# Performance work log

Measured on AMD Instinct MI355X. Metric: run time of the kernel, lower is better.

## Reference

```python
import jax, jax.numpy as jnp
import numpy as np

N = 50000   # num_nodes
E = 800000  # num_edges
IN, HID, OUT = 64, 96, 96
LN_EPS = 1e-5


def setup_inputs() -> dict:
    key = jax.random.key(0)
    ks = jax.random.split(key, 12)
    s = 0.05
    return {
        "x": jax.random.normal(ks[0], (N, IN), jnp.float32),
        "edge_index": jax.random.randint(ks[1], (2, E), 0, N, dtype=jnp.int64),
        "edge_weight": jax.random.uniform(ks[2], (E,), jnp.float32),
        "W0": jax.random.normal(ks[3], (IN, HID), jnp.float32) * s,
        "b0": jnp.zeros((HID,), jnp.float32),
        "ln_g": jnp.ones((HID,), jnp.float32),
        "ln_b": jnp.zeros((HID,), jnp.float32),
        "Ws": jax.random.normal(ks[4], (IN, HID), jnp.float32) * s,
        "bs": jnp.zeros((HID,), jnp.float32),
        "W1": jax.random.normal(ks[5], (HID, OUT), jnp.float32) * s,
        "b1": jnp.zeros((OUT,), jnp.float32),
    }


def _gcn(h, W, b, src, dst, ew, n):
    # GCNConv with add_self_loops=True and edge weights (PyG gcn_norm)
    loop = jnp.arange(n, dtype=src.dtype)
    s = jnp.concatenate([src, loop])
    d = jnp.concatenate([dst, loop])
    w = jnp.concatenate([ew, jnp.ones((n,), ew.dtype)])
    deg = jax.ops.segment_sum(w, d, num_segments=n)
    dinv = jnp.where(deg > 0, jax.lax.rsqrt(jnp.maximum(deg, 1e-12)), 0.0)
    norm = dinv[s] * w * dinv[d]                 # [E+N]
    msg = (h @ W)[s] * norm[:, None]             # gather transformed src feats
    return jax.ops.segment_sum(msg, d, num_segments=n) + b


def _layernorm(h, g, b):
    mu = h.mean(-1, keepdims=True)
    var = ((h - mu) ** 2).mean(-1, keepdims=True)
    return (h - mu) * jax.lax.rsqrt(var + LN_EPS) * g + b


def reference(x, edge_index, edge_weight, W0, b0, ln_g, ln_b, Ws, bs, W1, b1):
    src, dst = edge_index[0], edge_index[1]
    n = x.shape[0]
    # layer 0: GCN -> LayerNorm -> ReLU -> (dropout: eval no-op) -> +Linear skip
    h = _gcn(x, W0, b0, src, dst, edge_weight, n)
    h = jax.nn.relu(_layernorm(h, ln_g, ln_b))
    h = h + (x @ Ws + bs)
    # final layer: GCN only
    return _gcn(h, W1, b1, src, dst, edge_weight, n)
```

## Files before the change

### kernel.cpp

```cpp
#include <hip/hip_runtime.h>

#define LN_EPS 1e-5f

__device__ __forceinline__ float bflo(unsigned u) { union { unsigned u; float f; } c; c.u = u << 16; return c.f; }
__device__ __forceinline__ float bfhi(unsigned u) { union { unsigned u; float f; } c; c.u = u & 0xffff0000u; return c.f; }
__device__ __forceinline__ unsigned f2bfbits(float f) {
    union { float f; unsigned u; } c; c.f = f;
    return (c.u + 0x7fffu + ((c.u >> 16) & 1u)) >> 16;
}
__device__ __forceinline__ unsigned packbf(float lo, float hi) {
    return f2bfbits(lo) | (f2bfbits(hi) << 16);
}

__global__ void cnt_rank_kernel(const int* __restrict__ dst, int* __restrict__ cnt,
                                int* __restrict__ rank, int e) {
    int i = blockIdx.x * 256 + threadIdx.x;
    if (i >= e) return;
    rank[i] = atomicAdd(&cnt[dst[i]], 1);
}

__global__ void cvtprep_kernel(const float* __restrict__ x, unsigned* __restrict__ xb2, int total4,
                               const float* __restrict__ W0, const float* __restrict__ Ws,
                               const float* __restrict__ W1,
                               float4* __restrict__ w0i, float4* __restrict__ wsi,
                               float4* __restrict__ w1i, int* __restrict__ cnt,
                               int n, int gX) {
    int b = (int)blockIdx.x;
    if (b < gX) {
        int i = b * 256 + threadIdx.x;
        if (i >= total4) return;
        float4 v = ((const float4*)x)[i];
        uint2 o;
        o.x = packbf(v.x, v.y);
        o.y = packbf(v.z, v.w);
        ((uint2*)xb2)[i] = o;
    } else if (b < gX + 15) {
        int i = (b - gX) * 256 + threadIdx.x;
        if (i < 1536) {
            int kq = i / 96, j = i % 96;
            const float* p = W0 + kq * 4 * 96 + j;
            w0i[i] = make_float4(p[0], p[96], p[192], p[288]);
            const float* q = Ws + kq * 4 * 96 + j;
            wsi[i] = make_float4(q[0], q[96], q[192], q[288]);
        }
        int i2 = i - 1536;
        if (i2 >= 0 && i2 < 2304) {
            int kq = i2 / 96, j = i2 % 96;
            const float* p = W1 + kq * 4 * 96 + j;
            w1i[i2] = make_float4(p[0], p[96], p[192], p[288]);
        }
    } else {
        int i4 = ((b - gX - 15) * 256 + threadIdx.x) * 4;
        if (i4 + 3 < n) *(int4*)(cnt + i4) = make_int4(0, 0, 0, 0);
        else for (int k = i4; k < n; ++k) cnt[k] = 0;
    }
}

__global__ void blocksum_kernel(const int* __restrict__ cnt, int* __restrict__ bsum, int n) {
    int base = blockIdx.x * 1024;
    int t = threadIdx.x;
    int i0 = base + t * 4;
    int s = 0;
    if (i0 + 3 < n) { int4 v = *(const int4*)(cnt + i0); s = v.x + v.y + v.z + v.w; }
    else { for (int k = 0; k < 4; ++k) if (i0 + k < n) s += cnt[i0 + k]; }
    #pragma unroll
    for (int off = 32; off; off >>= 1) s += __shfl_xor(s, off);
    __shared__ int wsum[4];
    if ((t & 63) == 0) wsum[t >> 6] = s;
    __syncthreads();
    if (t == 0) bsum[blockIdx.x] = wsum[0] + wsum[1] + wsum[2] + wsum[3];
}

__global__ void scan_bsum_kernel(const int* __restrict__ bsum, int* __restrict__ boff, int nb) {
    int t = threadIdx.x;
    int carry = 0;
    for (int base = 0; base < nb; base += 64) {
        int i = base + t;
        int v = (i < nb) ? bsum[i] : 0;
        int sc = v;
        #pragma unroll
        for (int off = 1; off < 64; off <<= 1) {
            int u = __shfl_up(sc, off);
            if (t >= off) sc += u;
        }
        if (i < nb) boff[i] = carry + sc - v;
        carry += __shfl(sc, 63);
    }
}

__global__ void rowptr_kernel(const int* __restrict__ cnt, const int* __restrict__ boff,
                              int* __restrict__ rowptr, int n, int etot) {
    __shared__ int wsum[4];
    int b = blockIdx.x;
    int t = threadIdx.x;
    int i0 = b * 1024 + t * 4;
    int c0 = 0, c1 = 0, c2 = 0, c3 = 0;
    if (i0 < n)     c0 = cnt[i0];
    if (i0 + 1 < n) c1 = cnt[i0 + 1];
    if (i0 + 2 < n) c2 = cnt[i0 + 2];
    if (i0 + 3 < n) c3 = cnt[i0 + 3];
    int tot = c0 + c1 + c2 + c3;
    int lane = t & 63, w = t >> 6;
    int sc = tot;
    #pragma unroll
    for (int off = 1; off < 64; off <<= 1) {
        int u = __shfl_up(sc, off);
        if (lane >= off) sc += u;
    }
    if (lane == 63) wsum[w] = sc;
    __syncthreads();
    int woff = 0;
    for (int k = 0; k < w; ++k) woff += wsum[k];
    int excl = boff[b] + woff + sc - tot;
    if (i0 < n)     rowptr[i0]     = excl;
    if (i0 + 1 < n) rowptr[i0 + 1] = excl + c0;
    if (i0 + 2 < n) rowptr[i0 + 2] = excl + c0 + c1;
    if (i0 + 3 < n) rowptr[i0 + 3] = excl + c0 + c1 + c2;
    if (b == 0 && t == 0) rowptr[n] = etot;
}

__global__ void scatter_part_kernel(const int* __restrict__ src, const int* __restrict__ dst,
                                    const float* __restrict__ ew, const int* __restrict__ rank,
                                    const int* __restrict__ rowptr,
                                    uint2* __restrict__ cv, int e, int n) {
    int part = blockIdx.x & 7;
    int blk  = blockIdx.x >> 3;
    int chunk = (n + 7) >> 3;
    int lo = part * chunk;
    int hi = lo + chunk; if (hi > n) hi = n;
    int stride = (gridDim.x >> 3) * 256;
    for (int i = blk * 256 + threadIdx.x; i < e; i += stride) {
        int d = dst[i];
        if (d >= lo && d < hi) {
            int pos = rowptr[d] + rank[i];
            cv[pos] = make_uint2((unsigned)src[i], __float_as_uint(ew[i]));
        }
    }
}

__global__ void degsum_kernel(const int* __restrict__ rowptr, const uint2* __restrict__ cv,
                              float* __restrict__ dinv, int n) {
    int i = blockIdx.x * 256 + threadIdx.x;
    if (i >= n) return;
    int p0 = rowptr[i], p1 = rowptr[i + 1];
    float s = 1.0f;
    for (int p = p0; p < p1; ++p) s += __uint_as_float(cv[p].y);
    dinv[i] = rsqrtf(s);
}

__global__ void agg64_kernel(const unsigned* __restrict__ xb, const float* __restrict__ dinv,
                             const int* __restrict__ rowptr, const uint2* __restrict__ cv,
                             float* __restrict__ aggX, int n) {
    int node = blockIdx.x * 4 + (threadIdx.x >> 6);
    if (node >= n) return;
    int lane = threadIdx.x & 63;
    int g = lane >> 4, l4 = lane & 15;
    const uint2* x2 = (const uint2*)xb;
    int p0 = rowptr[node], pe = rowptr[node + 1];
    float a0 = 0, a1 = 0, a2 = 0, a3 = 0;
    float b0 = 0, b1 = 0, b2 = 0, b3 = 0;
    for (int p = p0 + g; p < pe; p += 8) {
        uint2 e1 = cv[p];
        int s1 = (int)e1.x;
        float w1 = __uint_as_float(e1.y) * dinv[s1];
        uint2 r1 = x2[(size_t)s1 * 16 + l4];
        bool h2 = (p + 4) < pe;
        uint2 e2 = h2 ? cv[p + 4] : e1;
        int s2 = (int)e2.x;
        float w2 = h2 ? __uint_as_float(e2.y) * dinv[s2] : 0.0f;
        uint2 r2 = x2[(size_t)s2 * 16 + l4];
        a0 = fmaf(w1, bflo(r1.x), a0); a1 = fmaf(w1, bfhi(r1.x), a1);
        a2 = fmaf(w1, bflo(r1.y), a2); a3 = fmaf(w1, bfhi(r1.y), a3);
        b0 = fmaf(w2, bflo(r2.x), b0); b1 = fmaf(w2, bfhi(r2.x), b1);
        b2 = fmaf(w2, bflo(r2.y), b2); b3 = fmaf(w2, bfhi(r2.y), b3);
    }
    a0 += b0; a1 += b1; a2 += b2; a3 += b3;
    #pragma unroll
    for (int off = 16; off <= 32; off <<= 1) {
        a0 += __shfl_xor(a0, off);
        a1 += __shfl_xor(a1, off);
        a2 += __shfl_xor(a2, off);
        a3 += __shfl_xor(a3, off);
    }
    if (g == 0) {
        float di = dinv[node];
        uint2 sr = x2[(size_t)node * 16 + l4];
        a0 = fmaf(di, bflo(sr.x), a0); a1 = fmaf(di, bfhi(sr.x), a1);
        a2 = fmaf(di, bflo(sr.y), a2); a3 = fmaf(di, bfhi(sr.y), a3);
        ((float4*)(aggX + (size_t)node * 64))[l4] =
            make_float4(a0 * di, a1 * di, a2 * di, a3 * di);
    }
}

__global__ __launch_bounds__(512) void gemm_ln_kernel(
        const float4* __restrict__ w0i, const float4* __restrict__ wsi,
        const float* __restrict__ aggX, const float* __restrict__ x,
        const float* __restrict__ b0,
        const float* __restrict__ ln_g, const float* __restrict__ ln_b,
        const float* __restrict__ bs,
        unsigned short* __restrict__ hb, int n) {
    __shared__ float4 w0s[1536];
    __shared__ float4 wss[1536];
    __shared__ float4 ar[1024];
    __shared__ float4 xr[1024];
    int t = threadIdx.x;
    int base = blockIdx.x * 64;
    for (int i = t; i < 1536; i += 512) { w0s[i] = w0i[i]; wss[i] = wsi[i]; }
    int rem = n - base; if (rem > 64) rem = 64;
    int nf4 = rem * 16;
    for (int i = t; i < nf4; i += 512) {
        ar[i] = ((const float4*)(aggX + (size_t)base * 64))[i];
        xr[i] = ((const float4*)(x + (size_t)base * 64))[i];
    }
    __syncthreads();
    int hw = t >> 5;
    int l = t & 31;
    int r0 = hw * 4;
    float acc[4][3] = {{0.f,0.f,0.f},{0.f,0.f,0.f},{0.f,0.f,0.f},{0.f,0.f,0.f}};
    float sk[4][3]  = {{0.f,0.f,0.f},{0.f,0.f,0.f},{0.f,0.f,0.f},{0.f,0.f,0.f}};
    for (int kq = 0; kq < 16; ++kq) {
        float4 wa = w0s[kq * 96 + l];
        float4 wb = w0s[kq * 96 + l + 32];
        float4 wc = w0s[kq * 96 + l + 64];
        float4 sa = wss[kq * 96 + l];
        float4 sb = wss[kq * 96 + l + 32];
        float4 scv = wss[kq * 96 + l + 64];
        #pragma unroll
        for (int r = 0; r < 4; ++r) {
            float4 a  = ar[(r0 + r) * 16 + kq];
            float4 xv = xr[(r0 + r) * 16 + kq];
            acc[r][0] = fmaf(a.w, wa.w, fmaf(a.z, wa.z, fmaf(a.y, wa.y, fmaf(a.x, wa.x, acc[r][0]))));
            acc[r][1] = fmaf(a.w, wb.w, fmaf(a.z, wb.z, fmaf(a.y, wb.y, fmaf(a.x, wb.x, acc[r][1]))));
            acc[r][2] = fmaf(a.w, wc.w, fmaf(a.z, wc.z, fmaf(a.y, wc.y, fmaf(a.x, wc.x, acc[r][2]))));
            sk[r][0]  = fmaf(xv.w, sa.w, fmaf(xv.z, sa.z, fmaf(xv.y, sa.y, fmaf(xv.x, sa.x, sk[r][0]))));
            sk[r][1]  = fmaf(xv.w, sb.w, fmaf(xv.z, sb.z, fmaf(xv.y, sb.y, fmaf(xv.x, sb.x, sk[r][1]))));
            sk[r][2]  = fmaf(xv.w, scv.w, fmaf(xv.z, scv.z, fmaf(xv.y, scv.y, fmaf(xv.x, scv.x, sk[r][2]))));
        }
    }
    float b00 = b0[l], b01 = b0[l + 32], b02 = b0[l + 64];
    float g0 = ln_g[l], g1 = ln_g[l + 32], g2 = ln_g[l + 64];
    float e0 = ln_b[l], e1 = ln_b[l + 32], e2 = ln_b[l + 64];
    float q0 = bs[l],   q1 = bs[l + 32],   q2 = bs[l + 64];
    #pragma unroll
    for (int r = 0; r < 4; ++r) {
        int node = base + r0 + r;
        if (node >= n) break;
        float a0v = acc[r][0] + b00, a1v = acc[r][1] + b01, a2v = acc[r][2] + b02;
        float s1 = a0v + a1v + a2v;
        #pragma unroll
        for (int off = 1; off < 32; off <<= 1) s1 += __shfl_xor(s1, off);
        float mu = s1 * (1.0f / 96.0f);
        float d0 = a0v - mu, d1 = a1v - mu, d2 = a2v - mu;
        float sq = d0 * d0 + d1 * d1 + d2 * d2;
        #pragma unroll
        for (int off = 1; off < 32; off <<= 1) sq += __shfl_xor(sq, off);
        float rinv = rsqrtf(sq * (1.0f / 96.0f) + LN_EPS);
        float v0 = fmaxf(d0 * rinv * g0 + e0, 0.0f) + sk[r][0] + q0;
        float v1 = fmaxf(d1 * rinv * g1 + e1, 0.0f) + sk[r][1] + q1;
        float v2 = fmaxf(d2 * rinv * g2 + e2, 0.0f) + sk[r][2] + q2;
        unsigned short* o = hb + (size_t)node * 96;
        o[l]      = (unsigned short)f2bfbits(v0);
        o[l + 32] = (unsigned short)f2bfbits(v1);
        o[l + 64] = (unsigned short)f2bfbits(v2);
    }
}

__global__ __launch_bounds__(1024) void agg96_out_kernel(
        const unsigned short* __restrict__ hb, const float* __restrict__ dinv,
        const int* __restrict__ rowptr, const uint2* __restrict__ cv,
        const float4* __restrict__ w1i, const float* __restrict__ b1,
        float* __restrict__ out, int n) {
    __shared__ float4 w1s[2304];
    __shared__ float4 hr[384];
    int t = threadIdx.x;
    for (int i = t; i < 2304; i += 1024) w1s[i] = w1i[i];
    int w = t >> 6;
    int node = blockIdx.x * 16 + w;
    int lane = t & 63;
    int g = lane >> 4, l4 = lane & 15;
    if (node < n) {
        const uint4* h4 = (const uint4*)hb;
        int p0 = rowptr[node], pe = rowptr[node + 1];
        float a0=0,a1=0,a2=0,a3=0,a4=0,a5=0,a6=0,a7=0;
        float c0=0,c1=0,c2=0,c3=0,c4=0,c5=0,c6=0,c7=0;
        if (l4 < 12) {
            for (int p = p0 + g; p < pe; p += 8) {
                uint2 e1 = cv[p];
                int s1 = (int)e1.x;
                float w1 = __uint_as_float(e1.y) * dinv[s1];
                uint4 r1 = h4[(size_t)s1 * 12 + l4];
                bool h2 = (p + 4) < pe;
                uint2 e2 = h2 ? cv[p + 4] : e1;
                int s2 = (int)e2.x;
                float w2 = h2 ? __uint_as_float(e2.y) * dinv[s2] : 0.0f;
                uint4 r2 = h4[(size_t)s2 * 12 + l4];
                a0 = fmaf(w1, bflo(r1.x), a0); a1 = fmaf(w1, bfhi(r1.x), a1);
                a2 = fmaf(w1, bflo(r1.y), a2); a3 = fmaf(w1, bfhi(r1.y), a3);
                a4 = fmaf(w1, bflo(r1.z), a4); a5 = fmaf(w1, bfhi(r1.z), a5);
                a6 = fmaf(w1, bflo(r1.w), a6); a7 = fmaf(w1, bfhi(r1.w), a7);
                c0 = fmaf(w2, bflo(r2.x), c0); c1 = fmaf(w2, bfhi(r2.x), c1);
                c2 = fmaf(w2, bflo(r2.y), c2); c3 = fmaf(w2, bfhi(r2.y), c3);
                c4 = fmaf(w2, bflo(r2.z), c4); c5 = fmaf(w2, bfhi(r2.z), c5);
                c6 = fmaf(w2, bflo(r2.w), c6); c7 = fmaf(w2, bfhi(r2.w), c7);
            }
            a0+=c0; a1+=c1; a2+=c2; a3+=c3; a4+=c4; a5+=c5; a6+=c6; a7+=c7;
        }
        #pragma unroll
        for (int off = 16; off <= 32; off <<= 1) {
            a0 += __shfl_xor(a0, off); a1 += __shfl_xor(a1, off);
            a2 += __shfl_xor(a2, off); a3 += __shfl_xor(a3, off);
            a4 += __shfl_xor(a4, off); a5 += __shfl_xor(a5, off);
            a6 += __shfl_xor(a6, off); a7 += __shfl_xor(a7, off);
        }
        if (g == 0 && l4 < 12) {
            float di = dinv[node];
            uint4 sr = h4[(size_t)node * 12 + l4];
            a0 = fmaf(di, bflo(sr.x), a0); a1 = fmaf(di, bfhi(sr.x), a1);
            a2 = fmaf(di, bflo(sr.y), a2); a3 = fmaf(di, bfhi(sr.y), a3);
            a4 = fmaf(di, bflo(sr.z), a4); a5 = fmaf(di, bfhi(sr.z), a5);
            a6 = fmaf(di, bflo(sr.w), a6); a7 = fmaf(di, bfhi(sr.w), a7);
            hr[w * 24 + l4 * 2]     = make_float4(a0 * di, a1 * di, a2 * di, a3 * di);
            hr[w * 24 + l4 * 2 + 1] = make_float4(a4 * di, a5 * di, a6 * di, a7 * di);
        }
    }
    __syncthreads();
    int g32 = t >> 5, l = t & 31;
    if (g32 < 24) {
        int rp = g32 / 3;
        int cb = g32 % 3;
        int colbase = cb * 32 + l;
        int r0 = rp * 2;
        float acc0 = 0.f, acc1 = 0.f;
        #pragma unroll 4
        for (int kq = 0; kq < 24; ++kq) {
            float4 wv = w1s[kq * 96 + colbase];
            float4 a0 = hr[r0 * 24 + kq];
            float4 a1 = hr[(r0 + 1) * 24 + kq];
            acc0 = fmaf(a0.w, wv.w, fmaf(a0.z, wv.z, fmaf(a0.y, wv.y, fmaf(a0.x, wv.x, acc0))));
            acc1 = fmaf(a1.w, wv.w, fmaf(a1.z, wv.z, fmaf(a1.y, wv.y, fmaf(a1.x, wv.x, acc1))));
        }
        float bb = b1[colbase];
        int n0 = blockIdx.x * 16 + r0;
        if (n0 < n)     out[(size_t)n0 * 96 + colbase]       = acc0 + bb;
        if (n0 + 1 < n) out[(size_t)(n0 + 1) * 96 + colbase] = acc1 + bb;
    }
}

extern "C" void kernel_launch(void* const* d_in, const int* in_sizes, int n_in,
                              void* d_out, int out_size, void* d_ws, size_t ws_size,
                              hipStream_t stream) {
    const float* x    = (const float*)d_in[0];
    const int*   ei   = (const int*)d_in[1];
    const float* ew   = (const float*)d_in[2];
    const float* W0   = (const float*)d_in[3];
    const float* b0   = (const float*)d_in[4];
    const float* ln_g = (const float*)d_in[5];
    const float* ln_b = (const float*)d_in[6];
    const float* Ws   = (const float*)d_in[7];
    const float* bs   = (const float*)d_in[8];
    const float* W1   = (const float*)d_in[9];
    const float* b1   = (const float*)d_in[10];
    float* out = (float*)d_out;

    const int E = in_sizes[2];
    const int N = in_sizes[0] / 64;
    const int* src = ei;
    const int* dst = ei + E;

    char* ws = (char*)d_ws;
    size_t off = 0;
    auto alloc = [&](size_t bytes) -> void* {
        void* p = ws + off;
        off = (off + bytes + 255) & ~(size_t)255;
        return p;
    };
    float* dinv   = (float*)alloc((size_t)N * 4);
    int*   cnt    = (int*)alloc((size_t)N * 4);
    int*   rowptr = (int*)alloc((size_t)(N + 1) * 4);
    int*   rank   = (int*)alloc((size_t)E * 4);
    int*   bsum   = (int*)alloc((size_t)256 * 4);
    int*   boff   = (int*)alloc((size_t)256 * 4);
    uint2* cv     = (uint2*)alloc((size_t)E * 8);
    unsigned* xb  = (unsigned*)alloc((size_t)N * 64 * 2);
    unsigned short* hb = (unsigned short*)alloc((size_t)N * 96 * 2);
    float* bufA   = (float*)alloc((size_t)N * 96 * 4);
    float4* w0i   = (float4*)alloc((size_t)1536 * 16);
    float4* wsi   = (float4*)alloc((size_t)1536 * 16);
    float4* w1i   = (float4*)alloc((size_t)2304 * 16);

    int gN = (N + 255) / 256;
    int gE = (E + 255) / 256;
    int nb = (N + 1023) / 1024;
    int gX = (N * 16 + 255) / 256;
    int gC = (N / 4 + 255) / 256;
    int gP = 8 * 128;

    cvtprep_kernel<<<gX + 15 + gC, 256, 0, stream>>>(x, xb, N * 16, W0, Ws, W1,
                                                     w0i, wsi, w1i, cnt, N, gX);
    cnt_rank_kernel<<<gE, 256, 0, stream>>>(dst, cnt, rank, E);
    blocksum_kernel<<<nb, 256, 0, stream>>>(cnt, bsum, N);
    scan_bsum_kernel<<<1, 64, 0, stream>>>(bsum, boff, nb);
    rowptr_kernel<<<nb, 256, 0, stream>>>(cnt, boff, rowptr, N, E);
    scatter_part_kernel<<<gP, 256, 0, stream>>>(src, dst, ew, rank, rowptr, cv, E, N);
    degsum_kernel<<<gN, 256, 0, stream>>>(rowptr, cv, dinv, N);

    int gA = (N + 3) / 4;
    agg64_kernel<<<gA, 256, 0, stream>>>(xb, dinv, rowptr, cv, bufA, N);

    int gG = (N + 63) / 64;
    gemm_ln_kernel<<<gG, 512, 0, stream>>>(w0i, wsi, bufA, x, b0, ln_g, ln_b, bs, hb, N);

    int gF = (N + 15) / 16;
    agg96_out_kernel<<<gF, 1024, 0, stream>>>(hb, dinv, rowptr, cv, w1i, b1, out, N);
}
```

Measured before the change: 211.2 us.

## Fuse layer-0 aggregation into GEMM+LayerNorm kernel and merge bf16 convert with counting

The layer-0 neighbour aggregation now runs inside the GEMM/LayerNorm kernel. 1024-thread blocks gather 64 nodes' aggregated features straight into shared memory, so the fp32 intermediate buffer no longer makes a global round trip. Separately, the x-to-bf16 conversion and the destination-count atomics are interleaved in one launch, and zeroing of the counts moves to its own small kernel. The costs are an extra launch, larger blocks with half the threads idle during the GEMM phase, and possibly lower occupancy from heavy shared memory use.

```diff
diff --git a/kernel.cpp b/kernel.cpp
--- a/kernel.cpp
+++ b/kernel.cpp
@@ -12,30 +12,37 @@
     return f2bfbits(lo) | (f2bfbits(hi) << 16);
 }
 
-__global__ void cnt_rank_kernel(const int* __restrict__ dst, int* __restrict__ cnt,
-                                int* __restrict__ rank, int e) {
-    int i = blockIdx.x * 256 + threadIdx.x;
-    if (i >= e) return;
-    rank[i] = atomicAdd(&cnt[dst[i]], 1);
-}
-
-__global__ void cvtprep_kernel(const float* __restrict__ x, unsigned* __restrict__ xb2, int total4,
-                               const float* __restrict__ W0, const float* __restrict__ Ws,
-                               const float* __restrict__ W1,
-                               float4* __restrict__ w0i, float4* __restrict__ wsi,
-                               float4* __restrict__ w1i, int* __restrict__ cnt,
-                               int n, int gX) {
+__global__ void zero_kernel(int* __restrict__ cnt, int n) {
+    int i4 = (blockIdx.x * 256 + threadIdx.x) * 4;
+    if (i4 + 3 < n) *(int4*)(cnt + i4) = make_int4(0, 0, 0, 0);
+    else for (int k = i4; k < n; ++k) cnt[k] = 0;
+}
+
+__global__ void cvtcnt_kernel(const float* __restrict__ x, unsigned* __restrict__ xb2, int total4,
+                              const int* __restrict__ dst, int* __restrict__ cnt,
+                              int* __restrict__ rank, int e,
+                              const float* __restrict__ W0, const float* __restrict__ Ws,
+                              const float* __restrict__ W1,
+                              float4* __restrict__ w0i, float4* __restrict__ wsi,
+                              float4* __restrict__ w1i, int gM) {
     int b = (int)blockIdx.x;
-    if (b < gX) {
-        int i = b * 256 + threadIdx.x;
-        if (i >= total4) return;
-        float4 v = ((const float4*)x)[i];
-        uint2 o;
-        o.x = packbf(v.x, v.y);
-        o.y = packbf(v.z, v.w);
-        ((uint2*)xb2)[i] = o;
-    } else if (b < gX + 15) {
-        int i = (b - gX) * 256 + threadIdx.x;
+    if (b < 2 * gM) {
+        int idx = b >> 1;
+        if ((b & 1) == 0) {
+            int i = idx * 256 + threadIdx.x;
+            if (i >= total4) return;
+            float4 v = ((const float4*)x)[i];
+            uint2 o;
+            o.x = packbf(v.x, v.y);
+            o.y = packbf(v.z, v.w);
+            ((uint2*)xb2)[i] = o;
+        } else {
+            int i = idx * 256 + threadIdx.x;
+            if (i >= e) return;
+            rank[i] = atomicAdd(&cnt[dst[i]], 1);
+        }
+    } else {
+        int i = (b - 2 * gM) * 256 + threadIdx.x;
         if (i < 1536) {
             int kq = i / 96, j = i % 96;
             const float* p = W0 + kq * 4 * 96 + j;
@@ -49,10 +56,6 @@
             const float* p = W1 + kq * 4 * 96 + j;
             w1i[i2] = make_float4(p[0], p[96], p[192], p[288]);
         }
-    } else {
-        int i4 = ((b - gX - 15) * 256 + threadIdx.x) * 4;
-        if (i4 + 3 < n) *(int4*)(cnt + i4) = make_int4(0, 0, 0, 0);
-        else for (int k = i4; k < n; ++k) cnt[k] = 0;
     }
 }
 
@@ -148,53 +151,11 @@
     dinv[i] = rsqrtf(s);
 }
 
-__global__ void agg64_kernel(const unsigned* __restrict__ xb, const float* __restrict__ dinv,
-                             const int* __restrict__ rowptr, const uint2* __restrict__ cv,
-                             float* __restrict__ aggX, int n) {
-    int node = blockIdx.x * 4 + (threadIdx.x >> 6);
-    if (node >= n) return;
-    int lane = threadIdx.x & 63;
-    int g = lane >> 4, l4 = lane & 15;
-    const uint2* x2 = (const uint2*)xb;
-    int p0 = rowptr[node], pe = rowptr[node + 1];
-    float a0 = 0, a1 = 0, a2 = 0, a3 = 0;
-    float b0 = 0, b1 = 0, b2 = 0, b3 = 0;
-    for (int p = p0 + g; p < pe; p += 8) {
-        uint2 e1 = cv[p];
-        int s1 = (int)e1.x;
-        float w1 = __uint_as_float(e1.y) * dinv[s1];
-        uint2 r1 = x2[(size_t)s1 * 16 + l4];
-        bool h2 = (p + 4) < pe;
-        uint2 e2 = h2 ? cv[p + 4] : e1;
-        int s2 = (int)e2.x;
-        float w2 = h2 ? __uint_as_float(e2.y) * dinv[s2] : 0.0f;
-        uint2 r2 = x2[(size_t)s2 * 16 + l4];
-        a0 = fmaf(w1, bflo(r1.x), a0); a1 = fmaf(w1, bfhi(r1.x), a1);
-        a2 = fmaf(w1, bflo(r1.y), a2); a3 = fmaf(w1, bfhi(r1.y), a3);
-        b0 = fmaf(w2, bflo(r2.x), b0); b1 = fmaf(w2, bfhi(r2.x), b1);
-        b2 = fmaf(w2, bflo(r2.y), b2); b3 = fmaf(w2, bfhi(r2.y), b3);
-    }
-    a0 += b0; a1 += b1; a2 += b2; a3 += b3;
-    #pragma unroll
-    for (int off = 16; off <= 32; off <<= 1) {
-        a0 += __shfl_xor(a0, off);
-        a1 += __shfl_xor(a1, off);
-        a2 += __shfl_xor(a2, off);
-        a3 += __shfl_xor(a3, off);
-    }
-    if (g == 0) {
-        float di = dinv[node];
-        uint2 sr = x2[(size_t)node * 16 + l4];
-        a0 = fmaf(di, bflo(sr.x), a0); a1 = fmaf(di, bfhi(sr.x), a1);
-        a2 = fmaf(di, bflo(sr.y), a2); a3 = fmaf(di, bfhi(sr.y), a3);
-        ((float4*)(aggX + (size_t)node * 64))[l4] =
-            make_float4(a0 * di, a1 * di, a2 * di, a3 * di);
-    }
-}
-
-__global__ __launch_bounds__(512) void gemm_ln_kernel(
+__global__ __launch_bounds__(1024) void agg64_ln_kernel(
+        const unsigned* __restrict__ xb, const float* __restrict__ dinv,
+        const int* __restrict__ rowptr, const uint2* __restrict__ cv,
         const float4* __restrict__ w0i, const float4* __restrict__ wsi,
-        const float* __restrict__ aggX, const float* __restrict__ x,
+        const float* __restrict__ x,
         const float* __restrict__ b0,
         const float* __restrict__ ln_g, const float* __restrict__ ln_b,
         const float* __restrict__ bs,
@@ -205,14 +166,59 @@
     __shared__ float4 xr[1024];
     int t = threadIdx.x;
     int base = blockIdx.x * 64;
-    for (int i = t; i < 1536; i += 512) { w0s[i] = w0i[i]; wss[i] = wsi[i]; }
+    for (int i = t; i < 1536; i += 1024) { w0s[i] = w0i[i]; wss[i] = wsi[i]; }
     int rem = n - base; if (rem > 64) rem = 64;
     int nf4 = rem * 16;
-    for (int i = t; i < nf4; i += 512) {
-        ar[i] = ((const float4*)(aggX + (size_t)base * 64))[i];
+    for (int i = t; i < nf4; i += 1024)
         xr[i] = ((const float4*)(x + (size_t)base * 64))[i];
+
+    int w = t >> 6;
+    int lane = t & 63;
+    int g = lane >> 4, l4 = lane & 15;
+    const uint2* x2 = (const uint2*)xb;
+    #pragma unroll
+    for (int rr = 0; rr < 4; ++rr) {
+        int nl = w * 4 + rr;
+        int node = base + nl;
+        if (node < n) {
+            int p0 = rowptr[node], pe = rowptr[node + 1];
+            float a0 = 0, a1 = 0, a2 = 0, a3 = 0;
+            float b0v = 0, b1v = 0, b2v = 0, b3v = 0;
+            for (int p = p0 + g; p < pe; p += 8) {
+                uint2 e1 = cv[p];
+                int s1 = (int)e1.x;
+                float w1 = __uint_as_float(e1.y) * dinv[s1];
+                uint2 r1 = x2[(size_t)s1 * 16 + l4];
+                bool h2 = (p + 4) < pe;
+                uint2 e2 = h2 ? cv[p + 4] : e1;
+                int s2 = (int)e2.x;
+                float w2 = h2 ? __uint_as_float(e2.y) * dinv[s2] : 0.0f;
+                uint2 r2 = x2[(size_t)s2 * 16 + l4];
+                a0 = fmaf(w1, bflo(r1.x), a0); a1 = fmaf(w1, bfhi(r1.x), a1);
+                a2 = fmaf(w1, bflo(r1.y), a2); a3 = fmaf(w1, bfhi(r1.y), a3);
+                b0v = fmaf(w2, bflo(r2.x), b0v); b1v = fmaf(w2, bfhi(r2.x), b1v);
+                b2v = fmaf(w2, bflo(r2.y), b2v); b3v = fmaf(w2, bfhi(r2.y), b3v);
+            }
+            a0 += b0v; a1 += b1v; a2 += b2v; a3 += b3v;
+            #pragma unroll
+            for (int off = 16; off <= 32; off <<= 1) {
+                a0 += __shfl_xor(a0, off);
+                a1 += __shfl_xor(a1, off);
+                a2 += __shfl_xor(a2, off);
+                a3 += __shfl_xor(a3, off);
+            }
+            if (g == 0) {
+                float di = dinv[node];
+                uint2 sr = x2[(size_t)node * 16 + l4];
+                a0 = fmaf(di, bflo(sr.x), a0); a1 = fmaf(di, bfhi(sr.x), a1);
+                a2 = fmaf(di, bflo(sr.y), a2); a3 = fmaf(di, bfhi(sr.y), a3);
+                ar[nl * 16 + l4] = make_float4(a0 * di, a1 * di, a2 * di, a3 * di);
+            }
+        }
     }
     __syncthreads();
+
+    if (t >= 512) return;
     int hw = t >> 5;
     int l = t & 31;
     int r0 = hw * 4;
@@ -383,7 +389,6 @@
     uint2* cv     = (uint2*)alloc((size_t)E * 8);
     unsigned* xb  = (unsigned*)alloc((size_t)N * 64 * 2);
     unsigned short* hb = (unsigned short*)alloc((size_t)N * 96 * 2);
-    float* bufA   = (float*)alloc((size_t)N * 96 * 4);
     float4* w0i   = (float4*)alloc((size_t)1536 * 16);
     float4* wsi   = (float4*)alloc((size_t)1536 * 16);
     float4* w1i   = (float4*)alloc((size_t)2304 * 16);
@@ -393,22 +398,21 @@
     int nb = (N + 1023) / 1024;
     int gX = (N * 16 + 255) / 256;
     int gC = (N / 4 + 255) / 256;
+    int gM = gX > gE ? gX : gE;
     int gP = 8 * 128;
 
-    cvtprep_kernel<<<gX + 15 + gC, 256, 0, stream>>>(x, xb, N * 16, W0, Ws, W1,
-                                                     w0i, wsi, w1i, cnt, N, gX);
-    cnt_rank_kernel<<<gE, 256, 0, stream>>>(dst, cnt, rank, E);
+    zero_kernel<<<gC, 256, 0, stream>>>(cnt, N);
+    cvtcnt_kernel<<<2 * gM + 15, 256, 0, stream>>>(x, xb, N * 16, dst, cnt, rank, E,
+                                                   W0, Ws, W1, w0i, wsi, w1i, gM);
     blocksum_kernel<<<nb, 256, 0, stream>>>(cnt, bsum, N);
     scan_bsum_kernel<<<1, 64, 0, stream>>>(bsum, boff, nb);
     rowptr_kernel<<<nb, 256, 0, stream>>>(cnt, boff, rowptr, N, E);
     scatter_part_kernel<<<gP, 256, 0, stream>>>(src, dst, ew, rank, rowptr, cv, E, N);
     degsum_kernel<<<gN, 256, 0, stream>>>(rowptr, cv, dinv, N);
 
-    int gA = (N + 3) / 4;
-    agg64_kernel<<<gA, 256, 0, stream>>>(xb, dinv, rowptr, cv, bufA, N);
-
-    int gG = (N + 63) / 64;
-    gemm_ln_kernel<<<gG, 512, 0, stream>>>(w0i, wsi, bufA, x, b0, ln_g, ln_b, bs, hb, N);
+    int gGL = (N + 63) / 64;
+    agg64_ln_kernel<<<gGL, 1024, 0, stream>>>(xb, dinv, rowptr, cv, w0i, wsi, x,
+                                              b0, ln_g, ln_b, bs, hb, N);
 
     int gF = (N + 15) / 16;
     agg96_out_kernel<<<gF, 1024, 0, stream>>>(hb, dinv, rowptr, cv, w1i, b1, out, N);
```

Result: slower. 241.8 us (+14.5%).
